# Optimization experiments

Hardware: AMD Instinct MI355X
Metric: run time of the kernel (lower is better)

Reference implementation:

```python
import jax, jax.numpy as jnp
import numpy as np

B = 16384   # number of cells
SD = 1024   # spatial_dim
TD = 1024   # temporal_dim
FD = 1024   # fusion_dim
H = 8       # num_attention_heads


def setup_inputs() -> dict:
    key = jax.random.key(0)
    ks = jax.random.split(key, 40)
    it = iter(range(40))

    def w(o, i):
        return jax.random.normal(ks[next(it)], (o, i), dtype=jnp.float32) * 0.02

    def b(o):
        return jnp.zeros((o,), dtype=jnp.float32)

    d = {
        "spatial_features": jax.random.normal(ks[next(it)], (B, SD), dtype=jnp.float32),
        "temporal_features": jax.random.normal(ks[next(it)], (B, TD), dtype=jnp.float32),
        "sp_w": w(FD, SD), "sp_b": b(FD),
        "tp_w": w(FD, TD), "tp_b": b(FD),
    }
    for pre in ("st", "ts", "sa"):  # spatial->temporal, temporal->spatial, self
        for nm in ("q", "k", "v", "o"):
            d[f"{pre}_{nm}w"] = w(FD, FD)
            d[f"{pre}_{nm}b"] = b(FD)
    d["f1_w"] = w(FD, 2 * FD); d["f1_b"] = b(FD)
    d["f2_w"] = w(FD, FD);     d["f2_b"] = b(FD)
    d["ln_g"] = jnp.ones((FD,), jnp.float32)
    d["ln_b"] = jnp.zeros((FD,), jnp.float32)
    return d


def _mha(xq, xk, xv, qw, qb, kw, kb, vw, vb, ow, ob):
    # xq: [B, Lq, D]; xk/xv: [B, Lk, D]
    Bx, Lq, D = xq.shape
    Lk = xk.shape[1]
    hd = D // H
    Q = (xq @ qw.T + qb).reshape(Bx, Lq, H, hd)
    K = (xk @ kw.T + kb).reshape(Bx, Lk, H, hd)
    V = (xv @ vw.T + vb).reshape(Bx, Lk, H, hd)
    scores = jnp.einsum("bqhd,bkhd->bhqk", Q, K) / jnp.sqrt(jnp.float32(hd))
    attn = jax.nn.softmax(scores, axis=-1)
    out = jnp.einsum("bhqk,bkhd->bqhd", attn, V).reshape(Bx, Lq, D)
    return out @ ow.T + ob


def reference(spatial_features, temporal_features,
              sp_w, sp_b, tp_w, tp_b,
              st_qw, st_qb, st_kw, st_kb, st_vw, st_vb, st_ow, st_ob,
              ts_qw, ts_qb, ts_kw, ts_kb, ts_vw, ts_vb, ts_ow, ts_ob,
              sa_qw, sa_qb, sa_kw, sa_kb, sa_vw, sa_vb, sa_ow, sa_ob,
              f1_w, f1_b, f2_w, f2_b, ln_g, ln_b):
    # projections to fusion dim, add seq_len=1 axis
    sp = (spatial_features @ sp_w.T + sp_b)[:, None, :]   # [B,1,F]
    tp = (temporal_features @ tp_w.T + tp_b)[:, None, :]  # [B,1,F]

    # cross attention
    s_att = _mha(sp, tp, tp, st_qw, st_qb, st_kw, st_kb, st_vw, st_vb, st_ow, st_ob)[:, 0, :]
    t_att = _mha(tp, sp, sp, ts_qw, ts_qb, ts_kw, ts_kb, ts_vw, ts_vb, ts_ow, ts_ob)[:, 0, :]

    # concat fusion MLP
    cat = jnp.concatenate([s_att, t_att], axis=-1)        # [B,2F]
    fused = jax.nn.relu(cat @ f1_w.T + f1_b) @ f2_w.T + f2_b

    # self attention over seq_len=1
    fe = fused[:, None, :]
    fused = _mha(fe, fe, fe, sa_qw, sa_qb, sa_kw, sa_kb, sa_vw, sa_vb, sa_ow, sa_ob)[:, 0, :]

    # layer norm (eps matches torch default 1e-5)
    mu = jnp.mean(fused, axis=-1, keepdims=True)
    var = jnp.mean(jnp.square(fused - mu), axis=-1, keepdims=True)
    return (fused - mu) * jax.lax.rsqrt(var + 1e-5) * ln_g + ln_b
```

## Files before the change

### kernel.cpp

```cpp
#include <hip/hip_runtime.h>
#include <hip/hip_fp16.h>


typedef _Float16 half8 __attribute__((ext_vector_type(8)));
typedef float floatx4 __attribute__((ext_vector_type(4)));

#define GLOBAL_AS __attribute__((address_space(1)))
#define LDS_AS __attribute__((address_space(3)))

#define NB 16384
#define FDIM 1024

#define SBAR() asm volatile("s_barrier" ::: "memory")
#define WAIT_LGKM0() asm volatile("s_waitcnt lgkmcnt(0)" ::: "memory")
#define WAIT_VM(n) asm volatile("s_waitcnt vmcnt(" #n ")" ::: "memory")
#define DSREAD(dst, addr) asm volatile("ds_read_b128 %0, %1" : "=v"(dst) : "v"(addr))

template <int RELU>
__global__ __launch_bounds__(512, 2) void gemm256(
    const _Float16* __restrict__ A, const _Float16* __restrict__ W,
    const float* __restrict__ bias, _Float16* __restrict__ C,
    int M, int N, int K, int ldc) {
  __shared__ __align__(16) _Float16 smem[2 * 2 * 256 * 64];

  const int t = threadIdx.x;
  const int lane = t & 63;
  const int w = t >> 6;
  const int wr = w >> 2;
  const int wc = w & 3;

  const int nwg = gridDim.x;
  const int bid = blockIdx.x;
  const int swz = (bid & 7) * (nwg >> 3) + (bid >> 3);
  const int nTN = N >> 8;
  const int m0 = (swz / nTN) << 8;
  const int n0 = (swz % nTN) << 8;
  const int NT = K >> 6;

  const int srow = w * 16 + (lane >> 3);
  const int scs = (lane & 7) ^ ((lane >> 3) & 7);
  const char* gA = (const char*)(A + (long)(m0 + srow) * K + scs * 8);
  const char* gB = (const char*)(W + (long)(n0 + srow) * K + scs * 8);
  const long dJ = (long)K * 16;
  const long dH = (long)K * 256;
  const int ldst = w * 2048 + lane * 16;

  unsigned sb = (unsigned)(unsigned long long)(LDS_AS void*)smem;
  const int frow = lane & 15;
  const unsigned offk = (unsigned)((((lane >> 4) * 16) ^ ((frow & 7) << 4)));
  const unsigned aoff = (unsigned)((wr * 128 + frow) * 128);
  const unsigned boff = (unsigned)(32768 + (wc * 64 + frow) * 128);

  floatx4 acc[8][4] = {};

#define STAGE(ab, h, buf, gp, kb)                                               \
  do {                                                                          \
    const char* _s = (gp) + (h) * dH + (kb);                                    \
    char* _d = (char*)smem + (buf) * 65536 + (ab) * 32768 + (h) * 16384 + ldst; \
    __builtin_amdgcn_global_load_lds((const GLOBAL_AS void*)_s,                 \
                                     (LDS_AS void*)_d, 16, 0, 0);               \
    __builtin_amdgcn_global_load_lds((const GLOBAL_AS void*)(_s + dJ),          \
                                     (LDS_AS void*)(_d + 1024), 16, 0, 0);      \
  } while (0)

#define QUAD(a0, a1, i0, i1)                                                              \
  do {                                                                                    \
    __builtin_amdgcn_s_setprio(1);                                                       \
    _Pragma("unroll") for (int c = 0; c < 4; ++c) {                                      \
      acc[i0][c] = __builtin_amdgcn_mfma_f32_16x16x32_f16(a0[0], b[c][0], acc[i0][c], 0, 0, 0); \
      acc[i0][c] = __builtin_amdgcn_mfma_f32_16x16x32_f16(a0[1], b[c][1], acc[i0][c], 0, 0, 0); \
      acc[i1][c] = __builtin_amdgcn_mfma_f32_16x16x32_f16(a1[0], b[c][0], acc[i1][c], 0, 0, 0); \
      acc[i1][c] = __builtin_amdgcn_mfma_f32_16x16x32_f16(a1[1], b[c][1], acc[i1][c], 0, 0, 0); \
    }                                                                                     \
    __builtin_amdgcn_s_setprio(0);                                                       \
  } while (0)

  {
    const long k1 = (NT > 1 ? 1 : 0) * 128L;
    STAGE(0, 0, 0, gA, 0); STAGE(0, 1, 0, gA, 0);
    STAGE(1, 0, 0, gB, 0); STAGE(1, 1, 0, gB, 0);
    STAGE(1, 0, 1, gB, k1); STAGE(0, 0, 1, gA, k1); STAGE(0, 1, 1, gA, k1);
  }
  WAIT_VM(6);
  SBAR();

  for (int kt = 0; kt < NT; ++kt) {
    const int cur = kt & 1, nxt = cur ^ 1;
    const unsigned baseA = sb + (unsigned)(cur * 65536) + aoff;
    const unsigned baseB = sb + (unsigned)(cur * 65536) + boff;
    const long kb1 = (long)(kt + 1 < NT ? kt + 1 : NT - 1) * 128;
    const long kb2 = (long)(kt + 2 < NT ? kt + 2 : NT - 1) * 128;

    half8 b[4][2], alo[4][2], ahi[4][2];

#pragma unroll
    for (int c = 0; c < 4; ++c) {
      DSREAD(b[c][0], baseB + c * 2048 + offk);
      DSREAD(b[c][1], baseB + c * 2048 + (offk ^ 64u));
    }
#pragma unroll
    for (int r = 0; r < 4; ++r) {
      DSREAD(alo[r][0], baseA + r * 2048 + offk);
      DSREAD(alo[r][1], baseA + r * 2048 + (offk ^ 64u));
    }
    STAGE(1, 1, nxt, gB, kb1);
    SBAR();
    WAIT_LGKM0();
    __builtin_amdgcn_sched_barrier(0);
    QUAD(alo[0], alo[1], 0, 1);
    SBAR();

#pragma unroll
    for (int r = 0; r < 4; ++r) {
      DSREAD(ahi[r][0], baseA + (r + 4) * 2048 + offk);
      DSREAD(ahi[r][1], baseA + (r + 4) * 2048 + (offk ^ 64u));
    }
    STAGE(1, 0, cur, gB, kb2);
    SBAR();
    WAIT_LGKM0();
    __builtin_amdgcn_sched_barrier(0);
    QUAD(alo[2], alo[3], 2, 3);
    SBAR();

    STAGE(0, 0, cur, gA, kb2);
    SBAR();
    __builtin_amdgcn_sched_barrier(0);
    QUAD(ahi[0], ahi[1], 4, 5);
    SBAR();

    STAGE(0, 1, cur, gA, kb2);
    WAIT_VM(6);
    SBAR();
    __builtin_amdgcn_sched_barrier(0);
    QUAD(ahi[2], ahi[3], 6, 7);
    SBAR();
  }
  WAIT_VM(0);

  const int rbase = (lane >> 4) * 4;
#pragma unroll
  for (int c = 0; c < 4; ++c) {
    const int col = n0 + wc * 64 + c * 16 + frow;
    const float bv = bias[col];
#pragma unroll
    for (int r = 0; r < 8; ++r) {
#pragma unroll
      for (int j = 0; j < 4; ++j) {
        int row = m0 + wr * 128 + r * 16 + rbase + j;
        float v = acc[r][c][j] + bv;
        if (RELU) v = fmaxf(v, 0.f);
        C[(long)row * ldc + col] = (_Float16)v;
      }
    }
  }
#undef STAGE
#undef QUAD
}

__global__ __launch_bounds__(256) void cvt_strided(const float* __restrict__ in, long ld_in,
                                                   _Float16* __restrict__ out, long ld_out,
                                                   long n4) {
  long i = (long)blockIdx.x * blockDim.x + threadIdx.x;
  long stride = (long)gridDim.x * blockDim.x;
  for (; i < n4; i += stride) {
    long row = i >> 8;
    long c4 = i & 255;
    float4 v = *reinterpret_cast<const float4*>(in + row * ld_in + c4 * 4);
    union { _Float16 h[4]; short4 s; } u;
    u.h[0] = (_Float16)v.x; u.h[1] = (_Float16)v.y;
    u.h[2] = (_Float16)v.z; u.h[3] = (_Float16)v.w;
    *reinterpret_cast<short4*>(out + row * ld_out + c4 * 4) = u.s;
  }
}

struct TP8 { const float* in[8]; _Float16* out[8]; };
__global__ __launch_bounds__(256) void transpose_cvt(TP8 args) {
  __shared__ float tile[32][33];
  const float* in = args.in[blockIdx.z];
  _Float16* out = args.out[blockIdx.z];
  const int bx = blockIdx.x * 32;
  const int by = blockIdx.y * 32;
  const int tx = threadIdx.x & 31;
  const int ty = threadIdx.x >> 5;
#pragma unroll
  for (int r = 0; r < 32; r += 8)
    tile[ty + r][tx] = in[(long)(by + ty + r) * 1024 + bx + tx];
  __syncthreads();
#pragma unroll
  for (int r = 0; r < 32; r += 8)
    out[(long)(bx + ty + r) * 1024 + by + tx] = (_Float16)tile[tx][ty + r];
}

struct MV3 {
  const float* W[3]; const float* x[3]; const float* add[3]; float* y[3]; long ld[3];
};
__global__ __launch_bounds__(256) void matvec3(MV3 a) {
  const int b = blockIdx.y;
  const int row = blockIdx.x * 4 + (threadIdx.x >> 6);
  const int lane = threadIdx.x & 63;
  const float* wr = a.W[b] + (long)row * a.ld[b];
  const float* xv = a.x[b];
  float s = 0.f;
#pragma unroll
  for (int j = 0; j < 4; ++j) {
    float4 w4 = *reinterpret_cast<const float4*>(wr + (lane + 64 * j) * 4);
    float4 x4 = *reinterpret_cast<const float4*>(xv + (lane + 64 * j) * 4);
    s += w4.x * x4.x + w4.y * x4.y + w4.z * x4.z + w4.w * x4.w;
  }
#pragma unroll
  for (int off = 32; off > 0; off >>= 1) s += __shfl_down(s, off);
  if (lane == 0) {
    const float* ad = a.add[b];
    a.y[b][row] = s + (ad ? ad[row] : 0.f);
  }
}

struct GemmArgs { const _Float16* A; const _Float16* W; const float* bias; _Float16* C; int ldc; };
struct GB5 { GemmArgs g[5]; };

__global__ __launch_bounds__(256, 2) void gemm_f16(GB5 args, int M, int N, int K) {
  __shared__ __align__(16) _Float16 As[128 * 32];
  __shared__ __align__(16) _Float16 Ws[128 * 32];

  const GemmArgs ga = args.g[blockIdx.y];
  const int t = threadIdx.x;
  const int lane = t & 63;
  const int wave = t >> 6;
  const int wr = wave >> 1;
  const int wc = wave & 1;

  const int nwg = gridDim.x;
  const int bid = blockIdx.x;
  const int swz = (bid & 7) * (nwg >> 3) + (bid >> 3);
  const int nTilesN = N >> 7;
  const int m0 = (swz / nTilesN) << 7;
  const int n0 = (swz % nTilesN) << 7;

  floatx4 acc[4][4] = {};
  const int srow = t >> 2;
  const int scol = (t & 3) * 8;
  const _Float16* Ag = ga.A + (long)(m0 + srow) * K + scol;
  const _Float16* Wg = ga.W + (long)(n0 + srow) * K + scol;
  const int frow = lane & 15;
  const int fk = (lane >> 4) * 8;

  for (int k0 = 0; k0 < K; k0 += 32) {
#pragma unroll
    for (int i = 0; i < 2; ++i) {
      __builtin_amdgcn_global_load_lds(
          (const GLOBAL_AS void*)(Ag + (long)i * 64 * K + k0),
          (LDS_AS void*)(&As[i * 2048 + t * 8]), 16, 0, 0);
      __builtin_amdgcn_global_load_lds(
          (const GLOBAL_AS void*)(Wg + (long)i * 64 * K + k0),
          (LDS_AS void*)(&Ws[i * 2048 + t * 8]), 16, 0, 0);
    }
    __syncthreads();
    half8 a[4], b[4];
#pragma unroll
    for (int r = 0; r < 4; ++r)
      a[r] = *(const half8*)&As[(wr * 64 + r * 16 + frow) * 32 + fk];
#pragma unroll
    for (int c = 0; c < 4; ++c)
      b[c] = *(const half8*)&Ws[(wc * 64 + c * 16 + frow) * 32 + fk];
#pragma unroll
    for (int r = 0; r < 4; ++r)
#pragma unroll
      for (int c = 0; c < 4; ++c)
        acc[r][c] = __builtin_amdgcn_mfma_f32_16x16x32_f16(a[r], b[c], acc[r][c], 0, 0, 0);
    __syncthreads();
  }

  const int rbase = lane >> 4;
#pragma unroll
  for (int c = 0; c < 4; ++c) {
    const int col = n0 + wc * 64 + c * 16 + frow;
    const float bv = ga.bias ? ga.bias[col] : 0.f;
#pragma unroll
    for (int r = 0; r < 4; ++r)
#pragma unroll
      for (int j = 0; j < 4; ++j) {
        int row = m0 + wr * 64 + r * 16 + rbase * 4 + j;
        ga.C[(long)row * ga.ldc + col] = (_Float16)(acc[r][c][j] + bv);
      }
  }
}

__global__ __launch_bounds__(256) void ln_f16(const _Float16* __restrict__ x,
                                              const float* __restrict__ g,
                                              const float* __restrict__ b,
                                              float* __restrict__ out) {
  const int row = blockIdx.x;
  const int t = threadIdx.x;
  const _Float16* xr = x + (size_t)row * FDIM;
  short4 raw = reinterpret_cast<const short4*>(xr)[t];
  union { short4 s; _Float16 h[4]; } u;
  u.s = raw;
  float v0 = (float)u.h[0], v1 = (float)u.h[1], v2 = (float)u.h[2], v3 = (float)u.h[3];
  float s = v0 + v1 + v2 + v3;
  float q = v0 * v0 + v1 * v1 + v2 * v2 + v3 * v3;
#pragma unroll
  for (int off = 32; off > 0; off >>= 1) {
    s += __shfl_down(s, off);
    q += __shfl_down(q, off);
  }
  __shared__ float ss[4], qs[4];
  int wave = t >> 6, lane = t & 63;
  if (lane == 0) { ss[wave] = s; qs[wave] = q; }
  __syncthreads();
  float S = ss[0] + ss[1] + ss[2] + ss[3];
  float Q = qs[0] + qs[1] + qs[2] + qs[3];
  float mu = S * (1.f / FDIM);
  float var = Q * (1.f / FDIM) - mu * mu;
  float rs = rsqrtf(var + 1e-5f);
  int c = t * 4;
  float4 o;
  o.x = (v0 - mu) * rs * g[c + 0] + b[c + 0];
  o.y = (v1 - mu) * rs * g[c + 1] + b[c + 1];
  o.z = (v2 - mu) * rs * g[c + 2] + b[c + 2];
  o.w = (v3 - mu) * rs * g[c + 3] + b[c + 3];
  reinterpret_cast<float4*>(out + (size_t)row * FDIM)[t] = o;
}

extern "C" void kernel_launch(void* const* d_in, const int* in_sizes, int n_in,
                              void* d_out, int out_size, void* d_ws, size_t ws_size,
                              hipStream_t stream) {
  const float* spatial  = (const float*)d_in[0];
  const float* temporal = (const float*)d_in[1];
  const float* sp_w = (const float*)d_in[2];
  const float* sp_b = (const float*)d_in[3];
  const float* tp_w = (const float*)d_in[4];
  const float* tp_b = (const float*)d_in[5];
  const float* st_vw = (const float*)d_in[10];
  const float* st_vb = (const float*)d_in[11];
  const float* st_ow = (const float*)d_in[12];
  const float* st_ob = (const float*)d_in[13];
  const float* ts_vw = (const float*)d_in[18];
  const float* ts_vb = (const float*)d_in[19];
  const float* ts_ow = (const float*)d_in[20];
  const float* ts_ob = (const float*)d_in[21];
  const float* sa_vw = (const float*)d_in[26];
  const float* sa_vb = (const float*)d_in[27];
  const float* sa_ow = (const float*)d_in[28];
  const float* sa_ob = (const float*)d_in[29];
  const float* f1_w = (const float*)d_in[30];
  const float* f1_b = (const float*)d_in[31];
  const float* f2_w = (const float*)d_in[32];
  const float* f2_b = (const float*)d_in[33];
  const float* ln_g = (const float*)d_in[34];
  const float* ln_b = (const float*)d_in[35];

  char* base = (char*)d_ws;
  size_t off = 0;
  auto alloc = [&](size_t bytes) { void* p = base + off; off += (bytes + 255) & ~255ull; return p; };
  const size_t W16 = 1024 * 1024 * sizeof(_Float16);

  _Float16* Xcat = (_Float16*)alloc((size_t)NB * 2048 * 2);
  _Float16* h    = (_Float16*)alloc((size_t)NB * 1024 * 2);
  _Float16* opre = (_Float16*)alloc((size_t)NB * 1024 * 2);
  _Float16* st_owT = (_Float16*)alloc(W16);
  _Float16* ts_owT = (_Float16*)alloc(W16);
  _Float16* sa_vwT = (_Float16*)alloc(W16);
  _Float16* tp_wT  = (_Float16*)alloc(W16);
  _Float16* sp_wT  = (_Float16*)alloc(W16);
  _Float16* f2_wT  = (_Float16*)alloc(W16);
  _Float16* f1a16  = (_Float16*)alloc(W16);
  _Float16* f1b16  = (_Float16*)alloc(W16);
  _Float16* sa_ow16= (_Float16*)alloc(W16);
  _Float16* st_vw16= (_Float16*)alloc(W16);
  _Float16* ts_vw16= (_Float16*)alloc(W16);
  _Float16* P1 = (_Float16*)alloc(W16);
  _Float16* Q2 = (_Float16*)alloc(W16);
  _Float16* P3 = (_Float16*)alloc(W16);
  _Float16* Q4 = (_Float16*)alloc(W16);
  _Float16* P5 = (_Float16*)alloc(W16);
  _Float16* W2 = (_Float16*)alloc(W16);
  _Float16* Wh = (_Float16*)alloc((size_t)1024 * 2048 * 2);
  float* u1 = (float*)alloc(3 * 1024 * 4);
  float* u2 = (float*)alloc(3 * 1024 * 4);
  float* bt = (float*)alloc(1024 * 4);
  float* bh = (float*)alloc(1024 * 4);

  cvt_strided<<<2048, 256, 0, stream>>>(temporal, 1024, Xcat, 2048, (long)NB * 256);
  cvt_strided<<<2048, 256, 0, stream>>>(spatial, 1024, Xcat + 1024, 2048, (long)NB * 256);

  TP8 tp = {};
  tp.in[0] = st_ow; tp.out[0] = st_owT;
  tp.in[1] = ts_ow; tp.out[1] = ts_owT;
  tp.in[2] = sa_vw; tp.out[2] = sa_vwT;
  tp.in[3] = tp_w;  tp.out[3] = tp_wT;
  tp.in[4] = sp_w;  tp.out[4] = sp_wT;
  tp.in[5] = f2_w;  tp.out[5] = f2_wT;
  transpose_cvt<<<dim3(32, 32, 6), 256, 0, stream>>>(tp);

  cvt_strided<<<1024, 256, 0, stream>>>(f1_w, 2048, f1a16, 1024, 1024 * 256);
  cvt_strided<<<1024, 256, 0, stream>>>(f1_w + 1024, 2048, f1b16, 1024, 1024 * 256);
  cvt_strided<<<1024, 256, 0, stream>>>(sa_ow, 1024, sa_ow16, 1024, 1024 * 256);
  cvt_strided<<<1024, 256, 0, stream>>>(st_vw, 1024, st_vw16, 1024, 1024 * 256);
  cvt_strided<<<1024, 256, 0, stream>>>(ts_vw, 1024, ts_vw16, 1024, 1024 * 256);

  {
    MV3 a;
    a.W[0] = st_vw; a.x[0] = tp_b; a.add[0] = st_vb; a.y[0] = u1;        a.ld[0] = 1024;
    a.W[1] = ts_vw; a.x[1] = sp_b; a.add[1] = ts_vb; a.y[1] = u1 + 1024; a.ld[1] = 1024;
    a.W[2] = sa_vw; a.x[2] = f2_b; a.add[2] = sa_vb; a.y[2] = u1 + 2048; a.ld[2] = 1024;
    matvec3<<<dim3(256, 3), 256, 0, stream>>>(a);
  }
  {
    MV3 a;
    a.W[0] = st_ow; a.x[0] = u1;        a.add[0] = st_ob; a.y[0] = u2;        a.ld[0] = 1024;
    a.W[1] = ts_ow; a.x[1] = u1 + 1024; a.add[1] = ts_ob; a.y[1] = u2 + 1024; a.ld[1] = 1024;
    a.W[2] = sa_ow; a.x[2] = u1 + 2048; a.add[2] = sa_ob; a.y[2] = u2 + 2048; a.ld[2] = 1024;
    matvec3<<<dim3(256, 3), 256, 0, stream>>>(a);
  }
  {
    MV3 a;
    a.W[0] = f1_w; a.x[0] = u2; a.add[0] = f1_b; a.y[0] = bt; a.ld[0] = 2048;
    matvec3<<<dim3(256, 1), 256, 0, stream>>>(a);
  }
  {
    MV3 a;
    a.W[0] = f1_w + 1024; a.x[0] = u2 + 1024; a.add[0] = bt; a.y[0] = bh; a.ld[0] = 2048;
    matvec3<<<dim3(256, 1), 256, 0, stream>>>(a);
  }

  {
    GB5 g = {};
    g.g[0] = { f1a16,  st_owT, nullptr, P1, 1024 };
    g.g[1] = { tp_wT,  st_vw16, nullptr, Q2, 1024 };
    g.g[2] = { f1b16,  ts_owT, nullptr, P3, 1024 };
    g.g[3] = { sp_wT,  ts_vw16, nullptr, Q4, 1024 };
    g.g[4] = { sa_ow16, sa_vwT, nullptr, P5, 1024 };
    gemm_f16<<<dim3(64, 5), 256, 0, stream>>>(g, 1024, 1024, 1024);
  }
  {
    GB5 g = {};
    g.g[0] = { P1, Q2, nullptr, Wh,        2048 };
    g.g[1] = { P3, Q4, nullptr, Wh + 1024, 2048 };
    g.g[2] = { P5, f2_wT, nullptr, W2,     1024 };
    gemm_f16<<<dim3(64, 3), 256, 0, stream>>>(g, 1024, 1024, 1024);
  }

  gemm256<1><<<dim3(256), 512, 0, stream>>>(Xcat, Wh, bh, h, NB, 1024, 2048, 1024);
  gemm256<0><<<dim3(256), 512, 0, stream>>>(h, W2, u2 + 2048, opre, NB, 1024, 1024, 1024);

  ln_f16<<<NB, 256, 0, stream>>>(opre, ln_g, ln_b, (float*)d_out);
}
```

Baseline: 247.6 us.

## Batch conversion and matvec launches, reorder GEMM A/B staging pipeline

Merges seven fp32→fp16 conversion launches into one batched kernel and collapses the two f1 matvecs into a single K=2048 matvec, reducing launch count. Also restructures the main GEMM's load schedule so that A tiles for the next step are prefetched during the current step and B tiles two steps ahead, with A fragment LDS reads split into halves interleaved with MFMA quads. The prologue now stages only B for step 1, and wait counts are adjusted to match. The cost is a different overlap balance in the hot GEMM, which could help or hurt.

```diff
diff --git a/kernel.cpp b/kernel.cpp
--- a/kernel.cpp
+++ b/kernel.cpp
@@ -53,14 +53,14 @@
 
   floatx4 acc[8][4] = {};
 
-#define STAGE(ab, h, buf, gp, kb)                                               \
-  do {                                                                          \
-    const char* _s = (gp) + (h) * dH + (kb);                                    \
-    char* _d = (char*)smem + (buf) * 65536 + (ab) * 32768 + (h) * 16384 + ldst; \
-    __builtin_amdgcn_global_load_lds((const GLOBAL_AS void*)_s,                 \
-                                     (LDS_AS void*)_d, 16, 0, 0);               \
-    __builtin_amdgcn_global_load_lds((const GLOBAL_AS void*)(_s + dJ),          \
-                                     (LDS_AS void*)(_d + 1024), 16, 0, 0);      \
+#define STAGE(ab, hf, buf, gp, kb)                                               \
+  do {                                                                           \
+    const char* _s = (gp) + (hf) * dH + (kb);                                    \
+    char* _d = (char*)smem + (buf) * 65536 + (ab) * 32768 + (hf) * 16384 + ldst; \
+    __builtin_amdgcn_global_load_lds((const GLOBAL_AS void*)_s,                  \
+                                     (LDS_AS void*)_d, 16, 0, 0);                \
+    __builtin_amdgcn_global_load_lds((const GLOBAL_AS void*)(_s + dJ),           \
+                                     (LDS_AS void*)(_d + 1024), 16, 0, 0);       \
   } while (0)
 
 #define QUAD(a0, a1, i0, i1)                                                              \
@@ -76,12 +76,12 @@
   } while (0)
 
   {
-    const long k1 = (NT > 1 ? 1 : 0) * 128L;
+    const long k1 = 128L;
     STAGE(0, 0, 0, gA, 0); STAGE(0, 1, 0, gA, 0);
     STAGE(1, 0, 0, gB, 0); STAGE(1, 1, 0, gB, 0);
-    STAGE(1, 0, 1, gB, k1); STAGE(0, 0, 1, gA, k1); STAGE(0, 1, 1, gA, k1);
-  }
-  WAIT_VM(6);
+    STAGE(1, 0, 1, gB, k1); STAGE(1, 1, 1, gB, k1);
+  }
+  WAIT_VM(4);
   SBAR();
 
   for (int kt = 0; kt < NT; ++kt) {
@@ -99,11 +99,11 @@
       DSREAD(b[c][1], baseB + c * 2048 + (offk ^ 64u));
     }
 #pragma unroll
-    for (int r = 0; r < 4; ++r) {
+    for (int r = 0; r < 2; ++r) {
       DSREAD(alo[r][0], baseA + r * 2048 + offk);
       DSREAD(alo[r][1], baseA + r * 2048 + (offk ^ 64u));
     }
-    STAGE(1, 1, nxt, gB, kb1);
+    STAGE(0, 0, nxt, gA, kb1);
     SBAR();
     WAIT_LGKM0();
     __builtin_amdgcn_sched_barrier(0);
@@ -111,26 +111,38 @@
     SBAR();
 
 #pragma unroll
-    for (int r = 0; r < 4; ++r) {
-      DSREAD(ahi[r][0], baseA + (r + 4) * 2048 + offk);
-      DSREAD(ahi[r][1], baseA + (r + 4) * 2048 + (offk ^ 64u));
-    }
-    STAGE(1, 0, cur, gB, kb2);
+    for (int r = 2; r < 4; ++r) {
+      DSREAD(alo[r][0], baseA + r * 2048 + offk);
+      DSREAD(alo[r][1], baseA + r * 2048 + (offk ^ 64u));
+    }
+    STAGE(0, 1, nxt, gA, kb1);
     SBAR();
     WAIT_LGKM0();
     __builtin_amdgcn_sched_barrier(0);
     QUAD(alo[2], alo[3], 2, 3);
     SBAR();
 
-    STAGE(0, 0, cur, gA, kb2);
-    SBAR();
+#pragma unroll
+    for (int r = 0; r < 2; ++r) {
+      DSREAD(ahi[r][0], baseA + (r + 4) * 2048 + offk);
+      DSREAD(ahi[r][1], baseA + (r + 4) * 2048 + (offk ^ 64u));
+    }
+    STAGE(1, 0, cur, gB, kb2);
+    SBAR();
+    WAIT_LGKM0();
     __builtin_amdgcn_sched_barrier(0);
     QUAD(ahi[0], ahi[1], 4, 5);
     SBAR();
 
-    STAGE(0, 1, cur, gA, kb2);
-    WAIT_VM(6);
-    SBAR();
+#pragma unroll
+    for (int r = 2; r < 4; ++r) {
+      DSREAD(ahi[r][0], baseA + (r + 4) * 2048 + offk);
+      DSREAD(ahi[r][1], baseA + (r + 4) * 2048 + (offk ^ 64u));
+    }
+    STAGE(1, 1, cur, gB, kb2);
+    WAIT_VM(4);
+    SBAR();
+    WAIT_LGKM0();
     __builtin_amdgcn_sched_barrier(0);
     QUAD(ahi[2], ahi[3], 6, 7);
     SBAR();
@@ -157,19 +169,20 @@
 #undef QUAD
 }
 
-__global__ __launch_bounds__(256) void cvt_strided(const float* __restrict__ in, long ld_in,
-                                                   _Float16* __restrict__ out, long ld_out,
-                                                   long n4) {
+struct CVE { const float* in; _Float16* out; long ld_in; long ld_out; long n4; };
+struct CVB { CVE e[7]; };
+__global__ __launch_bounds__(256) void cvt_batch(CVB a) {
+  const CVE e = a.e[blockIdx.y];
   long i = (long)blockIdx.x * blockDim.x + threadIdx.x;
   long stride = (long)gridDim.x * blockDim.x;
-  for (; i < n4; i += stride) {
+  for (; i < e.n4; i += stride) {
     long row = i >> 8;
     long c4 = i & 255;
-    float4 v = *reinterpret_cast<const float4*>(in + row * ld_in + c4 * 4);
+    float4 v = *reinterpret_cast<const float4*>(e.in + row * e.ld_in + c4 * 4);
     union { _Float16 h[4]; short4 s; } u;
     u.h[0] = (_Float16)v.x; u.h[1] = (_Float16)v.y;
     u.h[2] = (_Float16)v.z; u.h[3] = (_Float16)v.w;
-    *reinterpret_cast<short4*>(out + row * ld_out + c4 * 4) = u.s;
+    *reinterpret_cast<short4*>(e.out + row * e.ld_out + c4 * 4) = u.s;
   }
 }
 
@@ -191,28 +204,22 @@
     out[(long)(bx + ty + r) * 1024 + by + tx] = (_Float16)tile[tx][ty + r];
 }
 
-struct MV3 {
-  const float* W[3]; const float* x[3]; const float* add[3]; float* y[3]; long ld[3];
-};
-__global__ __launch_bounds__(256) void matvec3(MV3 a) {
-  const int b = blockIdx.y;
+struct MVE { const float* W; const float* x; const float* add; float* y; long ld; int kj; };
+struct MVB { MVE e[3]; };
+__global__ __launch_bounds__(256) void matvecb(MVB a) {
+  const MVE e = a.e[blockIdx.y];
   const int row = blockIdx.x * 4 + (threadIdx.x >> 6);
   const int lane = threadIdx.x & 63;
-  const float* wr = a.W[b] + (long)row * a.ld[b];
-  const float* xv = a.x[b];
+  const float* wr = e.W + (long)row * e.ld;
   float s = 0.f;
-#pragma unroll
-  for (int j = 0; j < 4; ++j) {
+  for (int j = 0; j < e.kj; ++j) {
     float4 w4 = *reinterpret_cast<const float4*>(wr + (lane + 64 * j) * 4);
-    float4 x4 = *reinterpret_cast<const float4*>(xv + (lane + 64 * j) * 4);
+    float4 x4 = *reinterpret_cast<const float4*>(e.x + (lane + 64 * j) * 4);
     s += w4.x * x4.x + w4.y * x4.y + w4.z * x4.z + w4.w * x4.w;
   }
 #pragma unroll
   for (int off = 32; off > 0; off >>= 1) s += __shfl_down(s, off);
-  if (lane == 0) {
-    const float* ad = a.add[b];
-    a.y[b][row] = s + (ad ? ad[row] : 0.f);
-  }
+  if (lane == 0) e.y[row] = s + (e.add ? e.add[row] : 0.f);
 }
 
 struct GemmArgs { const _Float16* A; const _Float16* W; const float* bias; _Float16* C; int ldc; };
@@ -377,11 +384,19 @@
   _Float16* Wh = (_Float16*)alloc((size_t)1024 * 2048 * 2);
   float* u1 = (float*)alloc(3 * 1024 * 4);
   float* u2 = (float*)alloc(3 * 1024 * 4);
-  float* bt = (float*)alloc(1024 * 4);
   float* bh = (float*)alloc(1024 * 4);
 
-  cvt_strided<<<2048, 256, 0, stream>>>(temporal, 1024, Xcat, 2048, (long)NB * 256);
-  cvt_strided<<<2048, 256, 0, stream>>>(spatial, 1024, Xcat + 1024, 2048, (long)NB * 256);
+  {
+    CVB cb = {};
+    cb.e[0] = { temporal, Xcat,        1024, 2048, (long)NB * 256 };
+    cb.e[1] = { spatial,  Xcat + 1024, 1024, 2048, (long)NB * 256 };
+    cb.e[2] = { f1_w,        f1a16,   2048, 1024, 1024 * 256 };
+    cb.e[3] = { f1_w + 1024, f1b16,   2048, 1024, 1024 * 256 };
+    cb.e[4] = { sa_ow,       sa_ow16, 1024, 1024, 1024 * 256 };
+    cb.e[5] = { st_vw,       st_vw16, 1024, 1024, 1024 * 256 };
+    cb.e[6] = { ts_vw,       ts_vw16, 1024, 1024, 1024 * 256 };
+    cvt_batch<<<dim3(1024, 7), 256, 0, stream>>>(cb);
+  }
 
   TP8 tp = {};
   tp.in[0] = st_ow; tp.out[0] = st_owT;
@@ -392,35 +407,24 @@
   tp.in[5] = f2_w;  tp.out[5] = f2_wT;
   transpose_cvt<<<dim3(32, 32, 6), 256, 0, stream>>>(tp);
 
-  cvt_strided<<<1024, 256, 0, stream>>>(f1_w, 2048, f1a16, 1024, 1024 * 256);
-  cvt_strided<<<1024, 256, 0, stream>>>(f1_w + 1024, 2048, f1b16, 1024, 1024 * 256);
-  cvt_strided<<<1024, 256, 0, stream>>>(sa_ow, 1024, sa_ow16, 1024, 1024 * 256);
-  cvt_strided<<<1024, 256, 0, stream>>>(st_vw, 1024, st_vw16, 1024, 1024 * 256);
-  cvt_strided<<<1024, 256, 0, stream>>>(ts_vw, 1024, ts_vw16, 1024, 1024 * 256);
-
-  {
-    MV3 a;
-    a.W[0] = st_vw; a.x[0] = tp_b; a.add[0] = st_vb; a.y[0] = u1;        a.ld[0] = 1024;
-    a.W[1] = ts_vw; a.x[1] = sp_b; a.add[1] = ts_vb; a.y[1] = u1 + 1024; a.ld[1] = 1024;
-    a.W[2] = sa_vw; a.x[2] = f2_b; a.add[2] = sa_vb; a.y[2] = u1 + 2048; a.ld[2] = 1024;
-    matvec3<<<dim3(256, 3), 256, 0, stream>>>(a);
-  }
-  {
-    MV3 a;
-    a.W[0] = st_ow; a.x[0] = u1;        a.add[0] = st_ob; a.y[0] = u2;        a.ld[0] = 1024;
-    a.W[1] = ts_ow; a.x[1] = u1 + 1024; a.add[1] = ts_ob; a.y[1] = u2 + 1024; a.ld[1] = 1024;
-    a.W[2] = sa_ow; a.x[2] = u1 + 2048; a.add[2] = sa_ob; a.y[2] = u2 + 2048; a.ld[2] = 1024;
-    matvec3<<<dim3(256, 3), 256, 0, stream>>>(a);
-  }
-  {
-    MV3 a;
-    a.W[0] = f1_w; a.x[0] = u2; a.add[0] = f1_b; a.y[0] = bt; a.ld[0] = 2048;
-    matvec3<<<dim3(256, 1), 256, 0, stream>>>(a);
-  }
-  {
-    MV3 a;
-    a.W[0] = f1_w + 1024; a.x[0] = u2 + 1024; a.add[0] = bt; a.y[0] = bh; a.ld[0] = 2048;
-    matvec3<<<dim3(256, 1), 256, 0, stream>>>(a);
+  {
+    MVB a = {};
+    a.e[0] = { st_vw, tp_b, st_vb, u1,        1024, 4 };
+    a.e[1] = { ts_vw, sp_b, ts_vb, u1 + 1024, 1024, 4 };
+    a.e[2] = { sa_vw, f2_b, sa_vb, u1 + 2048, 1024, 4 };
+    matvecb<<<dim3(256, 3), 256, 0, stream>>>(a);
+  }
+  {
+    MVB a = {};
+    a.e[0] = { st_ow, u1,        st_ob, u2,        1024, 4 };
+    a.e[1] = { ts_ow, u1 + 1024, ts_ob, u2 + 1024, 1024, 4 };
+    a.e[2] = { sa_ow, u1 + 2048, sa_ob, u2 + 2048, 1024, 4 };
+    matvecb<<<dim3(256, 3), 256, 0, stream>>>(a);
+  }
+  {
+    MVB a = {};
+    a.e[0] = { f1_w, u2, f1_b, bh, 2048, 8 };
+    matvecb<<<dim3(256, 1), 256, 0, stream>>>(a);
   }
 
   {
```

New measurement: 234.1 us. 5.5% less time.
